# Kernel tuning notes

Measured on AMD Instinct MI355X. Metric: run time of the kernel, lower is better.

The kernel has to match this reference:

```python
import jax, jax.numpy as jnp
import numpy as np

CHUNK = 1024  # matches CHUNK_SIZE in the torch module
DH = 8        # indexer_head_dim


def setup_inputs() -> dict:
    key0 = jax.random.key(0)
    ks = jax.random.split(key0, 5)
    D, H = 512, 4
    query = jax.random.normal(ks[0], (2, 4096, D), dtype=jnp.float32)
    key_t = jax.random.normal(ks[1], (2, 8192, D), dtype=jnp.float32)
    bound = 1.0 / np.sqrt(D)  # nn.Linear default init range
    Wq = jax.random.uniform(ks[2], (H * DH, D), minval=-bound, maxval=bound, dtype=jnp.float32)
    Wk = jax.random.uniform(ks[3], (H * DH, D), minval=-bound, maxval=bound, dtype=jnp.float32)
    output_weights = jax.random.normal(ks[4], (H,), dtype=jnp.float32)
    return {"query": query, "key": key_t, "Wq": Wq, "Wk": Wk,
            "output_weights": output_weights, "top_k": 64}


def reference(query, key, Wq, Wk, output_weights, top_k):
    B, NQ, _ = query.shape
    _, NK, _ = key.shape
    H = output_weights.shape[0]

    # projections -> [B, H, N, DH]
    q = (query @ Wq.T).reshape(B, NQ, H, DH).transpose(0, 2, 1, 3)
    k = (key @ Wk.T).reshape(B, NK, H, DH).transpose(0, 2, 1, 3)

    # per-(batch,head) symmetric int8 quantization (simulated in fp32, as the
    # original casts int8 back to float for the matmul)
    q_max = jnp.abs(q).max(axis=(2, 3), keepdims=True) + 1e-6
    k_max = jnp.abs(k).max(axis=(2, 3), keepdims=True) + 1e-6
    q_scale = q_max / 127.0
    k_scale = k_max / 127.0
    q_i = jnp.clip(jnp.round(q / q_scale), -127.0, 127.0)
    k_i = jnp.clip(jnp.round(k / k_scale), -127.0, 127.0)
    total_scale = q_scale * k_scale          # [B, H, 1, 1]
    w = output_weights.reshape(1, H, 1, 1)

    curr_k = min(top_k, NK)

    # chunk queries: [steps, B, H, CHUNK, DH] (NQ divisible by CHUNK)
    n_steps = NQ // CHUNK
    q_chunks = q_i.reshape(B, H, n_steps, CHUNK, DH).transpose(2, 0, 1, 3, 4)

    def step(carry, q_ch):
        # scores: [B, H, CHUNK, NK]
        s = jnp.einsum('bhcd,bhnd->bhcn', q_ch, k_i) * total_scale
        s = jax.nn.relu(s)
        reduced = (s * w).sum(axis=1)        # [B, CHUNK, NK]
        _, idx = jax.lax.top_k(reduced, curr_k)
        return carry, idx

    _, idxs = jax.lax.scan(step, None, q_chunks)  # [steps, B, CHUNK, curr_k]
    return idxs.transpose(1, 0, 2, 3).reshape(B, NQ, curr_k)
```

## Files before the change

kernel.cpp:

```cpp
#include <hip/hip_runtime.h>
#include <stdint.h>

#define BB 2
#define NQ 4096
#define NK 8192
#define DD 512
#define HH 4
#define TOPK 64
#define CAP 256
#define RPB 2
#define BLK 1024
#define HPAD 1088
#define SENT 0xFFFFFFFFu
#define ZBOUND 0x80000000FFFFFFFFull

typedef unsigned int u32;
typedef unsigned long long u64;

#if defined(__has_builtin)
#if __has_builtin(__builtin_amdgcn_sdot4)
#define HAVE_SDOT4 1
#endif
#endif

__device__ __forceinline__ int dot4i8(u32 a, u32 b, int acc) {
#ifdef HAVE_SDOT4
    return __builtin_amdgcn_sdot4((int)a, (int)b, acc, false);
#else
    acc += (int)(signed char)(a & 0xFF) * (int)(signed char)(b & 0xFF);
    acc += (int)(signed char)((a >> 8) & 0xFF) * (int)(signed char)((b >> 8) & 0xFF);
    acc += (int)(signed char)((a >> 16) & 0xFF) * (int)(signed char)((b >> 16) & 0xFF);
    acc += (int)(signed char)((a >> 24) & 0xFF) * (int)(signed char)((b >> 24) & 0xFF);
    return acc;
#endif
}


#define PROJ_BODY(EMIT)                                                          \
    __shared__ float4 xs[16][128];                                               \
    __shared__ float4 wl[128][16];                                               \
    const int nqrows = BB * NQ;                                                  \
    int blk = blockIdx.x;                                                        \
    int half = blk & 1;                                                          \
    int row0 = (blk >> 1) << 4;                                                  \
    int type = (row0 >= nqrows);                                                 \
    int trow0 = type ? row0 - nqrows : row0;                                     \
    int b = type ? (trow0 >> 13) : (trow0 >> 12);                                \
    const float* X = type ? key : query;                                         \
    const float* W = type ? Wk : Wq;                                             \
    const int t = threadIdx.x;                                                   \
    {                                                                            \
        const float4* xg = (const float4*)(X + (size_t)trow0 * DD);              \
        float4* xsf = &xs[0][0];                                                 \
        for (int i = t; i < 2048; i += 256) xsf[i] = xg[i];                      \
        const float4* wg = (const float4*)W;                                     \
        for (int i = t; i < 2048; i += 256) {                                    \
            int oo = i & 15, jj = i >> 4;                                        \
            wl[jj][oo] = wg[(size_t)(half * 16 + oo) * 128 + jj];                \
        }                                                                        \
    }                                                                            \
    __syncthreads();                                                             \
    int o16 = t & 15, lr = t >> 4;                                               \
    int o = half * 16 + o16;                                                     \
    int h = o >> 3;                                                              \
    int trow = trow0 + lr;                                                       \
    float acc0 = 0.f, acc1 = 0.f;                                                \
    _Pragma("unroll 8")                                                          \
    for (int j = 0; j < 128; ++j) {                                              \
        float4 a = xs[lr][j];                                                    \
        float4 bb = wl[j][o16];                                                  \
        acc0 = fmaf(a.x, bb.x, acc0);                                            \
        acc1 = fmaf(a.y, bb.y, acc1);                                            \
        acc0 = fmaf(a.z, bb.z, acc0);                                            \
        acc1 = fmaf(a.w, bb.w, acc1);                                            \
    }                                                                            \
    float v = acc0 + acc1;                                                       \
    EMIT

__global__ __launch_bounds__(256, 2) void proj_absmax_cached_kernel(
        const float* __restrict__ query, const float* __restrict__ key,
        const float* __restrict__ Wq, const float* __restrict__ Wk,
        u32* __restrict__ scale_bits,
        float* __restrict__ qf, float* __restrict__ kf) {
#pragma clang fp contract(off)
    __shared__ u32 lmax[4];
    if (threadIdx.x < 4) lmax[threadIdx.x] = 0u;
    PROJ_BODY(
        (type ? kf : qf)[(size_t)trow * 32 + o] = v;
        u32 bits = __float_as_uint(fabsf(v));
        __syncthreads();
        atomicMax(&lmax[h], bits);
        __syncthreads();
        if (threadIdx.x < 4 && lmax[threadIdx.x])
            atomicMax(&scale_bits[type * 8 + b * 4 + threadIdx.x], lmax[threadIdx.x]);
    )
}

__global__ __launch_bounds__(256, 2) void proj_absmax_kernel(
        const float* __restrict__ query, const float* __restrict__ key,
        const float* __restrict__ Wq, const float* __restrict__ Wk,
        u32* __restrict__ scale_bits) {
#pragma clang fp contract(off)
    __shared__ u32 lmax[4];
    if (threadIdx.x < 4) lmax[threadIdx.x] = 0u;
    PROJ_BODY(
        u32 bits = __float_as_uint(fabsf(v));
        __syncthreads();
        atomicMax(&lmax[h], bits);
        __syncthreads();
        if (threadIdx.x < 4 && lmax[threadIdx.x])
            atomicMax(&scale_bits[type * 8 + b * 4 + threadIdx.x], lmax[threadIdx.x]);
    )
}

__global__ __launch_bounds__(256) void quant_cached_kernel(
        const float* __restrict__ qf, const float* __restrict__ kf,
        const u32* __restrict__ scale_bits,
        char* __restrict__ q8, char* __restrict__ kp8) {
#pragma clang fp contract(off)
    const int nq = BB * NQ * 32;
    int gid = blockIdx.x * 256 + threadIdx.x;
    int type = (gid >= nq);
    int idx = type ? gid - nq : gid;
    int h = (idx >> 3) & 3;
    int b = type ? (idx >> 18) : (idx >> 17);
    float v = (type ? kf : qf)[idx];
    float mx = __uint_as_float(scale_bits[type * 8 + b * 4 + h]);
    float scale = (mx + 1e-6f) / 127.0f;
    float r = rintf(v / scale);
    r = fminf(fmaxf(r, -127.f), 127.f);
    (type ? kp8 : q8)[idx] = (char)(int)r;
}

__global__ __launch_bounds__(256, 2) void proj_quant_kernel(
        const float* __restrict__ query, const float* __restrict__ key,
        const float* __restrict__ Wq, const float* __restrict__ Wk,
        const u32* __restrict__ scale_bits,
        char* __restrict__ q8, char* __restrict__ kp8) {
#pragma clang fp contract(off)
    PROJ_BODY(
        float mx = __uint_as_float(scale_bits[type * 8 + b * 4 + h]);
        float scale = (mx + 1e-6f) / 127.0f;
        float r = rintf(v / scale);
        r = fminf(fmaxf(r, -127.f), 127.f);
        (type ? kp8 : q8)[(size_t)trow * 32 + o] = (char)(int)r;
    )
}

#define SCORE_U(r, udst) { \
    float acc = 0.f; \
    { int s = dot4i8(qa[r][0], c0.x, 0); s = dot4i8(qa[r][1], c0.y, s); \
      float sf = (float)s * tsr[r][0]; sf = fmaxf(sf, 0.f); \
      float pr = sf * wtr[0]; acc = acc + pr; } \
    { int s = dot4i8(qa[r][2], c0.z, 0); s = dot4i8(qa[r][3], c0.w, s); \
      float sf = (float)s * tsr[r][1]; sf = fmaxf(sf, 0.f); \
      float pr = sf * wtr[1]; acc = acc + pr; } \
    { int s = dot4i8(qa[r][4], c1.x, 0); s = dot4i8(qa[r][5], c1.y, s); \
      float sf = (float)s * tsr[r][2]; sf = fmaxf(sf, 0.f); \
      float pr = sf * wtr[2]; acc = acc + pr; } \
    { int s = dot4i8(qa[r][6], c1.z, 0); s = dot4i8(qa[r][7], c1.w, s); \
      float sf = (float)s * tsr[r][3]; sf = fmaxf(sf, 0.f); \
      float pr = sf * wtr[3]; acc = acc + pr; } \
    acc = acc + 0.0f; \
    u32 uu = __float_as_uint(acc); \
    udst = (uu & 0x80000000u) ? ~uu : (uu | 0x80000000u); }

#define SELECT_PASS(r, SHIFT, BINSN) do { \
    const int bpl_ = ((BINSN) >= 64) ? ((BINSN) / 64) : 1; \
    const int nact_ = ((BINSN) >= 64) ? 64 : (BINSN); \
    u32 P_ = 0u; \
    if (lane < nact_) { \
        for (int j_ = 0; j_ < bpl_; ++j_) { int bin_ = lane * bpl_ + j_; P_ += hist[r][bin_ + (bin_ >> 4)]; } } \
    u32 sI_ = P_; \
    for (int s_ = 1; s_ < 64; s_ <<= 1) { u32 o_ = __shfl_down(sI_, s_, 64); if (lane + s_ < 64) sI_ += o_; } \
    u32 sE_ = sI_ - P_; \
    u32 Gp_ = G_l[r]; \
    if (Gp_ + sE_ < TOPK && Gp_ + sI_ >= TOPK) { \
        u32 run_ = Gp_ + sE_; \
        for (int j_ = bpl_ - 1; j_ >= 0; --j_) { \
            int bin_ = lane * bpl_ + j_; u32 c_ = hist[r][bin_ + (bin_ >> 4)]; \
            if (run_ + c_ >= TOPK) { \
                T_l[r] |= ((u64)(u32)bin_) << (SHIFT); \
                G_l[r] = run_; cc_l[r] = run_ + c_; break; } \
            run_ += c_; } } \
} while (0)

__global__ __launch_bounds__(BLK) void score_topk_kernel(
    const char* __restrict__ q8, const char* __restrict__ kp8,
    const u32* __restrict__ scale_bits, const float* __restrict__ w,
    int* __restrict__ out) {
#pragma clang fp contract(off)
    __shared__ u32 scores[RPB][NK];
    __shared__ u32 hist[RPB][HPAD];
    __shared__ u64 cand[RPB][CAP];
    __shared__ u32 cnt[RPB];
    __shared__ u64 T_l[RPB];
    __shared__ u32 G_l[RPB], cc_l[RPB];

    const int blk = blockIdx.x;
    const int row0 = blk * RPB;
    const int b = row0 >> 12;
    const int t = threadIdx.x;
    const int lane = t & 63;
    const int wv = t >> 6;

    if (t < RPB) { cnt[t] = 0u; T_l[t] = 0ull; G_l[t] = 0u; cc_l[t] = SENT; }
    for (int i = t; i < RPB * HPAD; i += BLK) (&hist[0][0])[i] = 0u;

    u32 qa[RPB][8];
    float tsr[RPB][HH], wtr[HH];
#pragma unroll
    for (int r = 0; r < RPB; ++r) {
        const u32* qr = (const u32*)(q8 + (size_t)(row0 + r) * 32);
#pragma unroll
        for (int j = 0; j < 8; ++j) qa[r][j] = qr[j];
    }
#pragma unroll
    for (int h = 0; h < HH; ++h) {
        float qsc = (__uint_as_float(scale_bits[b * 4 + h]) + 1e-6f) / 127.0f;
        float ksc = (__uint_as_float(scale_bits[8 + b * 4 + h]) + 1e-6f) / 127.0f;
        float tsv = qsc * ksc;
#pragma unroll
        for (int r = 0; r < RPB; ++r) tsr[r][h] = tsv;
        wtr[h] = w[h];
    }
    __syncthreads();

    const u32* kbase = (const u32*)(kp8 + (size_t)b * NK * 32);

    for (int i = 0; i < NK / BLK; ++i) {
        int n = t + i * BLK;
        const u32* kr = kbase + (size_t)n * 8;
        uint4 c0 = *(const uint4*)(kr);
        uint4 c1 = *(const uint4*)(kr + 4);
#define DO_ROW(r) { u32 u; SCORE_U(r, u); scores[r][n] = u; \
        if (u > 0x80000000u) { u32 bin = u >> 22; \
            atomicAdd(&hist[r][bin + (bin >> 4)], 1u); } }
        DO_ROW(0) DO_ROW(1)
#undef DO_ROW
    }
    __syncthreads();
    if (wv < RPB) SELECT_PASS(wv, 54, 1024);
    __syncthreads();

    {
        bool f0 = (cc_l[0] == SENT) || (T_l[0] <= ZBOUND);
        bool f1 = (cc_l[1] == SENT) || (T_l[1] <= ZBOUND);
        if (f0 || f1) {
            if (t == 0) {
                if (f0) { T_l[0] = 0ull; G_l[0] = 0u; cc_l[0] = SENT; }
                if (f1) { T_l[1] = 0ull; G_l[1] = 0u; cc_l[1] = SENT; }
            }
            for (int i = t; i < RPB * HPAD; i += BLK) (&hist[0][0])[i] = 0u;
            __syncthreads();
            for (int i = 0; i < NK / BLK; ++i) {
                int n = t + i * BLK;
                if (f0) { u32 u = scores[0][n]; u32 bin = u >> 22;
                          atomicAdd(&hist[0][bin + (bin >> 4)], 1u); }
                if (f1) { u32 u = scores[1][n]; u32 bin = u >> 22;
                          atomicAdd(&hist[1][bin + (bin >> 4)], 1u); }
            }
            __syncthreads();
            if (wv == 0 && f0) SELECT_PASS(0, 54, 1024);
            if (wv == 1 && f1) SELECT_PASS(1, 54, 1024);
            __syncthreads();
        }
    }

    const int shifts[6] = {44, 34, 24, 14, 4, 0};
    for (int p = 0; p < 6; ++p) {
        __syncthreads();
        if (!((cc_l[0] > CAP) || (cc_l[1] > CAP))) break;
        const int shift = shifts[p];
        const int width = (shift == 0) ? 4 : 10;
        const u32 binmask = (1u << width) - 1u;
        const u64 himask = ~0ull << (shift + width);
        for (int i = t; i < RPB * HPAD; i += BLK) (&hist[0][0])[i] = 0u;
        __syncthreads();
        for (int i = 0; i < NK / BLK; ++i) {
            int n = t + i * BLK;
            u32 lo = 0xFFFFFFFFu - (u32)n;
#define DO_ROW(r) if (cc_l[r] > CAP) { \
            u64 kk = ((u64)scores[r][n] << 32) | (u64)lo; \
            if (((kk ^ T_l[r]) & himask) == 0ull) { \
                u32 bin = (u32)(kk >> shift) & binmask; \
                atomicAdd(&hist[r][bin + (bin >> 4)], 1u); } }
            DO_ROW(0) DO_ROW(1)
#undef DO_ROW
        }
        __syncthreads();
        if (wv < RPB && cc_l[wv] > CAP) {
            if (width == 10) SELECT_PASS(wv, shift, 1024);
            else             SELECT_PASS(wv, shift, 16);
        }
    }
    __syncthreads();

    for (int i = 0; i < NK / BLK; ++i) {
        int n = t + i * BLK;
        u32 lo = 0xFFFFFFFFu - (u32)n;
#define DO_ROW(r) { u64 kk = ((u64)scores[r][n] << 32) | (u64)lo; \
        if (kk >= T_l[r]) { u32 pos = atomicAdd(&cnt[r], 1u); \
            if (pos < CAP) cand[r][pos] = kk; } }
        DO_ROW(0) DO_ROW(1)
#undef DO_ROW
    }
    __syncthreads();
    for (int i = t; i < RPB * CAP; i += BLK) {
        int r = i >> 8, j = i & (CAP - 1);
        if ((u32)j >= cnt[r]) cand[r][j] = 0ull;
    }

    for (u32 k2 = 2; k2 <= CAP; k2 <<= 1) {
        for (u32 jj = k2 >> 1; jj > 0; jj >>= 1) {
            __syncthreads();
            if (t < RPB * CAP) {
                int r = t >> 8;
                u32 idx = (u32)(t & (CAP - 1));
                u32 partner = idx ^ jj;
                if (partner > idx) {
                    u64 a = cand[r][idx], d = cand[r][partner];
                    bool descBlock = ((idx & k2) == 0);
                    if (descBlock ? (a < d) : (a > d)) { cand[r][idx] = d; cand[r][partner] = a; }
                }
            }
        }
    }
    __syncthreads();

    if (t < RPB * TOPK) {
        int r = t >> 6, j = t & 63;
        out[(size_t)(row0 + r) * TOPK + j] = (int)(0xFFFFFFFFu - (u32)cand[r][j]);
    }
}

extern "C" void kernel_launch(void* const* d_in, const int* in_sizes, int n_in,
                              void* d_out, int out_size, void* d_ws, size_t ws_size,
                              hipStream_t stream) {
    const float* query = (const float*)d_in[0];
    const float* key = (const float*)d_in[1];
    const float* Wq = (const float*)d_in[2];
    const float* Wk = (const float*)d_in[3];
    const float* ow = (const float*)d_in[4];

    char* ws = (char*)d_ws;
    u32* scale_bits = (u32*)ws;
    char* q8 = ws + 1024;
    char* kp8 = q8 + BB * NQ * 32;
    float* qf = (float*)(ws + 1024 + 768 * 1024);
    float* kf = qf + BB * NQ * 32;
    int* out = (int*)d_out;

    (void)hipMemsetAsync(scale_bits, 0, 64, stream);

    const size_t need = 1024 + 768 * 1024 + 3 * 1024 * 1024;
    const int nblocks = (BB * (NQ + NK)) / 16 * 2;
    const int total_elems = BB * (NQ + NK) * 32;
    if (ws_size >= need) {
        proj_absmax_cached_kernel<<<nblocks, 256, 0, stream>>>(query, key, Wq, Wk,
                                                               scale_bits, qf, kf);
        quant_cached_kernel<<<total_elems / 256, 256, 0, stream>>>(qf, kf, scale_bits, q8, kp8);
    } else {
        proj_absmax_kernel<<<nblocks, 256, 0, stream>>>(query, key, Wq, Wk, scale_bits);
        proj_quant_kernel<<<nblocks, 256, 0, stream>>>(query, key, Wq, Wk, scale_bits, q8, kp8);
    }
    score_topk_kernel<<<(BB * NQ) / RPB, BLK, 0, stream>>>(q8, kp8, scale_bits, ow, out);
}
```

Measured before the change: 208.2 us.

## Compute scores with int8 MFMA over 16 query rows and recompute instead of storing

Adds a score/top-k kernel that uses int8 MFMA instructions to compute per-head scores for 16 query rows per block. Blocks are zero-masked per head so one MFMA output lane holds one head's dot product. Scores are no longer kept in shared memory. Each radix-select pass and the final candidate gather recompute them from the key matrix. This removes the per-row sdot4 work and the large shared score buffer, at the cost of rereading keys and redoing the matmul on every pass.

```diff
diff --git a/kernel.cpp b/kernel.cpp
--- a/kernel.cpp
+++ b/kernel.cpp
@@ -8,16 +8,28 @@
 #define HH 4
 #define TOPK 64
 #define CAP 256
-#define RPB 2
-#define BLK 1024
 #define HPAD 1088
 #define SENT 0xFFFFFFFFu
 #define ZBOUND 0x80000000FFFFFFFFull
 
+#define RPB 2
+#define BLK 1024
+#define RM 16
+#define SBLK 1024
+#define NWV 16
+
 typedef unsigned int u32;
 typedef unsigned long long u64;
+typedef int v4i __attribute__((ext_vector_type(4)));
 
 #if defined(__has_builtin)
+#if __has_builtin(__builtin_amdgcn_mfma_i32_16x16x32_i8)
+#define MFMA32 1
+#define USE_MFMA 1
+#elif __has_builtin(__builtin_amdgcn_mfma_i32_16x16x64_i8)
+#define MFMA64 1
+#define USE_MFMA 1
+#endif
 #if __has_builtin(__builtin_amdgcn_sdot4)
 #define HAVE_SDOT4 1
 #endif
@@ -147,24 +159,6 @@
     )
 }
 
-#define SCORE_U(r, udst) { \
-    float acc = 0.f; \
-    { int s = dot4i8(qa[r][0], c0.x, 0); s = dot4i8(qa[r][1], c0.y, s); \
-      float sf = (float)s * tsr[r][0]; sf = fmaxf(sf, 0.f); \
-      float pr = sf * wtr[0]; acc = acc + pr; } \
-    { int s = dot4i8(qa[r][2], c0.z, 0); s = dot4i8(qa[r][3], c0.w, s); \
-      float sf = (float)s * tsr[r][1]; sf = fmaxf(sf, 0.f); \
-      float pr = sf * wtr[1]; acc = acc + pr; } \
-    { int s = dot4i8(qa[r][4], c1.x, 0); s = dot4i8(qa[r][5], c1.y, s); \
-      float sf = (float)s * tsr[r][2]; sf = fmaxf(sf, 0.f); \
-      float pr = sf * wtr[2]; acc = acc + pr; } \
-    { int s = dot4i8(qa[r][6], c1.z, 0); s = dot4i8(qa[r][7], c1.w, s); \
-      float sf = (float)s * tsr[r][3]; sf = fmaxf(sf, 0.f); \
-      float pr = sf * wtr[3]; acc = acc + pr; } \
-    acc = acc + 0.0f; \
-    u32 uu = __float_as_uint(acc); \
-    udst = (uu & 0x80000000u) ? ~uu : (uu | 0x80000000u); }
-
 #define SELECT_PASS(r, SHIFT, BINSN) do { \
     const int bpl_ = ((BINSN) >= 64) ? ((BINSN) / 64) : 1; \
     const int nact_ = ((BINSN) >= 64) ? 64 : (BINSN); \
@@ -184,6 +178,258 @@
                 G_l[r] = run_; cc_l[r] = run_ + c_; break; } \
             run_ += c_; } } \
 } while (0)
+
+#ifdef USE_MFMA
+
+#ifdef MFMA32
+#define KTILE(kt) \
+    long long bq_ = *(const long long*)(kbase + ((size_t)((kt) * 16 + lc)) * 32 + lg * 8); \
+    v4i cA = __builtin_amdgcn_mfma_i32_16x16x32_i8(am0, bq_, vz, 0, 0, 0); \
+    v4i cB = __builtin_amdgcn_mfma_i32_16x16x32_i8(am1, bq_, vz, 0, 0, 0); \
+    v4i cC = __builtin_amdgcn_mfma_i32_16x16x32_i8(am2, bq_, vz, 0, 0, 0); \
+    v4i cD = __builtin_amdgcn_mfma_i32_16x16x32_i8(am3, bq_, vz, 0, 0, 0);
+#else
+#define KTILE(kt) \
+    v4i bq_ = vz; \
+    if (lg < 2) bq_ = *(const v4i*)(kbase + ((size_t)((kt) * 16 + lc)) * 32 + lg * 16); \
+    v4i cA = __builtin_amdgcn_mfma_i32_16x16x64_i8(am0, bq_, vz, 0, 0, 0); \
+    v4i cB = __builtin_amdgcn_mfma_i32_16x16x64_i8(am1, bq_, vz, 0, 0, 0); \
+    v4i cC = __builtin_amdgcn_mfma_i32_16x16x64_i8(am2, bq_, vz, 0, 0, 0); \
+    v4i cD = __builtin_amdgcn_mfma_i32_16x16x64_i8(am3, bq_, vz, 0, 0, 0);
+#endif
+
+#define SCORE_J(j, udst) { \
+    float acc_ = 0.f; \
+    { float sf_ = (float)cA[j] * tsr[0]; sf_ = fmaxf(sf_, 0.f); \
+      float pr_ = sf_ * wtr[0]; acc_ = acc_ + pr_; } \
+    { float sf_ = (float)cB[j] * tsr[1]; sf_ = fmaxf(sf_, 0.f); \
+      float pr_ = sf_ * wtr[1]; acc_ = acc_ + pr_; } \
+    { float sf_ = (float)cC[j] * tsr[2]; sf_ = fmaxf(sf_, 0.f); \
+      float pr_ = sf_ * wtr[2]; acc_ = acc_ + pr_; } \
+    { float sf_ = (float)cD[j] * tsr[3]; sf_ = fmaxf(sf_, 0.f); \
+      float pr_ = sf_ * wtr[3]; acc_ = acc_ + pr_; } \
+    acc_ = acc_ + 0.0f; \
+    u32 uu_ = __float_as_uint(acc_); \
+    udst = (uu_ & 0x80000000u) ? ~uu_ : (uu_ | 0x80000000u); }
+
+__global__ __attribute__((amdgpu_waves_per_eu(4, 4))) __launch_bounds__(SBLK)
+void score_topk_mfma_kernel(
+    const char* __restrict__ q8, const char* __restrict__ kp8,
+    const u32* __restrict__ scale_bits, const float* __restrict__ w,
+    int* __restrict__ out) {
+#pragma clang fp contract(off)
+    __shared__ u32 hist[RM][HPAD];
+    __shared__ u64 cand[RM][CAP];
+    __shared__ u32 cnt[RM];
+    __shared__ u64 T_l[RM];
+    __shared__ u32 G_l[RM], cc_l[RM], fbf[RM];
+    __shared__ u32 flagA, needs;
+
+    const int row0 = blockIdx.x * RM;
+    const int b = row0 >> 12;
+    const int t = threadIdx.x;
+    const int lane = t & 63;
+    const int wv = t >> 6;
+    const int lg = lane >> 4;
+    const int lc = lane & 15;
+    const v4i vz = {0, 0, 0, 0};
+
+    if (t < RM) { cnt[t] = 0u; T_l[t] = 0ull; G_l[t] = 0u; cc_l[t] = SENT; fbf[t] = 0u; }
+    for (int i = t; i < RM * HPAD; i += SBLK) (&hist[0][0])[i] = 0u;
+
+    float tsr[HH], wtr[HH];
+#pragma unroll
+    for (int h = 0; h < HH; ++h) {
+        float qsc = (__uint_as_float(scale_bits[b * 4 + h]) + 1e-6f) / 127.0f;
+        float ksc = (__uint_as_float(scale_bits[8 + b * 4 + h]) + 1e-6f) / 127.0f;
+        tsr[h] = qsc * ksc;
+        wtr[h] = w[h];
+    }
+
+#ifdef MFMA32
+    long long am0, am1, am2, am3;
+    {
+        const long long* qrow = (const long long*)(q8 + (size_t)(row0 + lc) * 32);
+        long long aq = qrow[lg];
+        am0 = (lg == 0) ? aq : 0ll;
+        am1 = (lg == 1) ? aq : 0ll;
+        am2 = (lg == 2) ? aq : 0ll;
+        am3 = (lg == 3) ? aq : 0ll;
+    }
+#else
+    v4i am0 = vz, am1 = vz, am2 = vz, am3 = vz;
+    {
+        const int* qrow = (const int*)(q8 + (size_t)(row0 + lc) * 32);
+        int w0 = 0, w1 = 0, w2 = 0, w3 = 0;
+        if (lg < 2) { w0 = qrow[lg * 4 + 0]; w1 = qrow[lg * 4 + 1];
+                      w2 = qrow[lg * 4 + 2]; w3 = qrow[lg * 4 + 3]; }
+        if (lg == 0) { am0.x = w0; am0.y = w1; am1.z = w2; am1.w = w3; }
+        if (lg == 1) { am2.x = w0; am2.y = w1; am3.z = w2; am3.w = w3; }
+    }
+#endif
+    __syncthreads();
+
+    const char* kbase = kp8 + (size_t)b * NK * 32;
+
+    for (int kt = wv; kt < NK / 16; kt += NWV) {
+        KTILE(kt);
+#pragma unroll
+        for (int j = 0; j < 4; ++j) {
+            u32 u; SCORE_J(j, u);
+            int row = (lg << 2) + j;
+            if (u > 0x80000000u) { u32 bin = u >> 22;
+                atomicAdd(&hist[row][bin + (bin >> 4)], 1u); }
+        }
+    }
+    __syncthreads();
+    SELECT_PASS(wv, 54, 1024);
+    __syncthreads();
+
+    if (t == 0) {
+        u32 a = 0;
+        for (int r = 0; r < RM; ++r) {
+            u32 f = (cc_l[r] == SENT || T_l[r] <= ZBOUND) ? 1u : 0u;
+            fbf[r] = f; a |= f;
+        }
+        flagA = a;
+    }
+    __syncthreads();
+    if (flagA) {
+        if (t < RM && fbf[t]) { T_l[t] = 0ull; G_l[t] = 0u; cc_l[t] = SENT; }
+        for (int i = t; i < RM * HPAD; i += SBLK) (&hist[0][0])[i] = 0u;
+        __syncthreads();
+        u32 f0 = fbf[(lg << 2) + 0], f1 = fbf[(lg << 2) + 1];
+        u32 f2 = fbf[(lg << 2) + 2], f3 = fbf[(lg << 2) + 3];
+        for (int kt = wv; kt < NK / 16; kt += NWV) {
+            KTILE(kt);
+#pragma unroll
+            for (int j = 0; j < 4; ++j) {
+                u32 fj = (j == 0) ? f0 : (j == 1) ? f1 : (j == 2) ? f2 : f3;
+                if (fj) {
+                    u32 u; SCORE_J(j, u);
+                    int row = (lg << 2) + j;
+                    u32 bin = u >> 22;
+                    atomicAdd(&hist[row][bin + (bin >> 4)], 1u);
+                }
+            }
+        }
+        __syncthreads();
+        if (fbf[wv]) SELECT_PASS(wv, 54, 1024);
+        __syncthreads();
+    }
+
+    const int shifts[6] = {44, 34, 24, 14, 4, 0};
+    for (int p = 0; p < 6; ++p) {
+        __syncthreads();
+        if (t == 0) {
+            u32 a = 0;
+            for (int r = 0; r < RM; ++r) a |= (cc_l[r] > CAP) ? 1u : 0u;
+            needs = a;
+        }
+        __syncthreads();
+        if (!needs) break;
+        const int shift = shifts[p];
+        const int width = (shift == 0) ? 4 : 10;
+        const u32 binmask = (1u << width) - 1u;
+        const u64 himask = ~0ull << (shift + width);
+        for (int i = t; i < RM * HPAD; i += SBLK) (&hist[0][0])[i] = 0u;
+        __syncthreads();
+        u64 T0 = T_l[(lg << 2) + 0], T1 = T_l[(lg << 2) + 1];
+        u64 T2 = T_l[(lg << 2) + 2], T3 = T_l[(lg << 2) + 3];
+        u32 g0 = cc_l[(lg << 2) + 0] > CAP, g1 = cc_l[(lg << 2) + 1] > CAP;
+        u32 g2 = cc_l[(lg << 2) + 2] > CAP, g3 = cc_l[(lg << 2) + 3] > CAP;
+        for (int kt = wv; kt < NK / 16; kt += NWV) {
+            KTILE(kt);
+            u32 lo = 0xFFFFFFFFu - (u32)(kt * 16 + lc);
+#pragma unroll
+            for (int j = 0; j < 4; ++j) {
+                u32 gj = (j == 0) ? g0 : (j == 1) ? g1 : (j == 2) ? g2 : g3;
+                if (gj) {
+                    u64 Tj = (j == 0) ? T0 : (j == 1) ? T1 : (j == 2) ? T2 : T3;
+                    u32 u; SCORE_J(j, u);
+                    u64 kk = ((u64)u << 32) | (u64)lo;
+                    if (((kk ^ Tj) & himask) == 0ull) {
+                        int row = (lg << 2) + j;
+                        u32 bin = (u32)(kk >> shift) & binmask;
+                        atomicAdd(&hist[row][bin + (bin >> 4)], 1u);
+                    }
+                }
+            }
+        }
+        __syncthreads();
+        if (cc_l[wv] > CAP) {
+            if (width == 10) SELECT_PASS(wv, shift, 1024);
+            else             SELECT_PASS(wv, shift, 16);
+        }
+    }
+    __syncthreads();
+
+    {
+        u64 T0 = T_l[(lg << 2) + 0], T1 = T_l[(lg << 2) + 1];
+        u64 T2 = T_l[(lg << 2) + 2], T3 = T_l[(lg << 2) + 3];
+        for (int kt = wv; kt < NK / 16; kt += NWV) {
+            KTILE(kt);
+            u32 lo = 0xFFFFFFFFu - (u32)(kt * 16 + lc);
+#pragma unroll
+            for (int j = 0; j < 4; ++j) {
+                u64 Tj = (j == 0) ? T0 : (j == 1) ? T1 : (j == 2) ? T2 : T3;
+                u32 u; SCORE_J(j, u);
+                u64 kk = ((u64)u << 32) | (u64)lo;
+                if (kk >= Tj) {
+                    int row = (lg << 2) + j;
+                    u32 pos = atomicAdd(&cnt[row], 1u);
+                    if (pos < CAP) cand[row][pos] = kk;
+                }
+            }
+        }
+    }
+    __syncthreads();
+    for (int i = t; i < RM * CAP; i += SBLK) {
+        int r = i >> 8, j = i & (CAP - 1);
+        if ((u32)j >= cnt[r]) cand[r][j] = 0ull;
+    }
+
+    for (u32 k2 = 2; k2 <= CAP; k2 <<= 1) {
+        for (u32 jj = k2 >> 1; jj > 0; jj >>= 1) {
+            __syncthreads();
+            for (int c = t; c < RM * CAP; c += SBLK) {
+                int r = c >> 8;
+                u32 idx = (u32)(c & (CAP - 1));
+                u32 partner = idx ^ jj;
+                if (partner > idx) {
+                    u64 a = cand[r][idx], d = cand[r][partner];
+                    bool descBlock = ((idx & k2) == 0);
+                    if (descBlock ? (a < d) : (a > d)) { cand[r][idx] = d; cand[r][partner] = a; }
+                }
+            }
+        }
+    }
+    __syncthreads();
+
+    if (t < RM * TOPK) {
+        int r = t >> 6, j = t & 63;
+        out[(size_t)(row0 + r) * TOPK + j] = (int)(0xFFFFFFFFu - (u32)cand[r][j]);
+    }
+}
+#endif
+
+#define SCORE_U(r, udst) { \
+    float acc = 0.f; \
+    { int s = dot4i8(qa[r][0], c0.x, 0); s = dot4i8(qa[r][1], c0.y, s); \
+      float sf = (float)s * tsr[r][0]; sf = fmaxf(sf, 0.f); \
+      float pr = sf * wtr[0]; acc = acc + pr; } \
+    { int s = dot4i8(qa[r][2], c0.z, 0); s = dot4i8(qa[r][3], c0.w, s); \
+      float sf = (float)s * tsr[r][1]; sf = fmaxf(sf, 0.f); \
+      float pr = sf * wtr[1]; acc = acc + pr; } \
+    { int s = dot4i8(qa[r][4], c1.x, 0); s = dot4i8(qa[r][5], c1.y, s); \
+      float sf = (float)s * tsr[r][2]; sf = fmaxf(sf, 0.f); \
+      float pr = sf * wtr[2]; acc = acc + pr; } \
+    { int s = dot4i8(qa[r][6], c1.z, 0); s = dot4i8(qa[r][7], c1.w, s); \
+      float sf = (float)s * tsr[r][3]; sf = fmaxf(sf, 0.f); \
+      float pr = sf * wtr[3]; acc = acc + pr; } \
+    acc = acc + 0.0f; \
+    u32 uu = __float_as_uint(acc); \
+    udst = (uu & 0x80000000u) ? ~uu : (uu | 0x80000000u); }
 
 __global__ __launch_bounds__(BLK) void score_topk_kernel(
     const char* __restrict__ q8, const char* __restrict__ kp8,
@@ -364,5 +610,9 @@
         proj_absmax_kernel<<<nblocks, 256, 0, stream>>>(query, key, Wq, Wk, scale_bits);
         proj_quant_kernel<<<nblocks, 256, 0, stream>>>(query, key, Wq, Wk, scale_bits, q8, kp8);
     }
+#ifdef USE_MFMA
+    score_topk_mfma_kernel<<<(BB * NQ) / RM, SBLK, 0, stream>>>(q8, kp8, scale_bits, ow, out);
+#else
     score_topk_kernel<<<(BB * NQ) / RPB, BLK, 0, stream>>>(q8, kp8, scale_bits, ow, out);
-}
+#endif
+}
```

New measurement: 208.8 us. About the same (+0.3%).
